# Performance work log

Hardware: AMD Instinct MI355X
Metric: run time of the kernel (lower is better)

## Reference

```python
import jax, jax.numpy as jnp
import numpy as np

P, N, E, H = 8192, 32, 256, 8
D = E // H
CUT_A, CUT_B = 0.001, 0.005  # self.length_range = (0.001, 0.005, None, None)
SQRT3 = 1.7320508075688772


def _soft_square_cutoff(x):
    # smooth ramp 0->1 on [CUT_A, CUT_B], 0 below, 1 above (high-side ranges are None)
    t = jnp.clip((x - CUT_A) / (CUT_B - CUT_A), 0.0, 1.0)
    return 0.5 * (1.0 - jnp.cos(jnp.pi * t))


def setup_inputs() -> dict:
    key = jax.random.key(0)
    ks = jax.random.split(key, 16)
    s = 1.0 / np.sqrt(E)
    inp = {
        "query": jax.random.normal(ks[0], (P, E), jnp.float32),
        "key_x": jax.random.normal(ks[1], (P, E), jnp.float32),
        "value": jax.random.normal(ks[2], (P, E), jnp.float32),
        "index_pair": jax.random.randint(ks[3], (P, N), 0, P),
        "relative_atten_weights": jax.random.normal(ks[4], (P, N, H), jnp.float32),
        # lengths ~ N(0, 0.002*sqrt(3)) so they span the (0.001, 0.005) cutoff range
        "rpe_distance": jax.random.normal(ks[5], (P, N, 3), jnp.float32) * 0.002,
        "Wq": jax.random.normal(ks[6], (E, E), jnp.float32) * s,
        "bq": jnp.zeros((E,), jnp.float32),
        "Wk": jax.random.normal(ks[7], (E, E), jnp.float32) * s,
        "bk": jnp.zeros((E,), jnp.float32),
        "Wv": jax.random.normal(ks[8], (E, E), jnp.float32) * s,
        "bv": jnp.zeros((E,), jnp.float32),
        "Wg1": jax.random.normal(ks[9], (E, 3 * H), jnp.float32) * s,
        "bg1": jnp.zeros((3 * H,), jnp.float32),
        "Wg2": jax.random.normal(ks[10], (3 * H, 3 * H), jnp.float32) * (1.0 / np.sqrt(3 * H)),
        "bg2": jnp.zeros((3 * H,), jnp.float32),
    }
    return inp


def reference(query, key_x, value, index_pair, relative_atten_weights, rpe_distance,
              Wq, bq, Wk, bk, Wv, bv, Wg1, bg1, Wg2, bg2):
    # --- RPE spherical harmonics (irreps 1x0e+1x1e, component norm); keep l=1 part ([:,1:])
    rlen = jnp.linalg.norm(rpe_distance, axis=-1, keepdims=True)        # [P,N,1]
    unit = rpe_distance / jnp.maximum(rlen, 1e-12)                      # normalize=True
    cutoff = _soft_square_cutoff(rlen)                                  # nonscalar cutoff
    rpe_edge_sh = SQRT3 * unit * cutoff                                 # [P,N,3]

    # --- projections
    q = query @ Wq + bq                                                 # [P,E]
    k = key_x @ Wk + bk
    v = value @ Wv + bv

    # --- mapper_v6: per-edge gather of key/value rows
    k_g = k[index_pair]                                                 # [P,N,E]
    v_g = v[index_pair]                                                 # [P,N,E]

    # --- dot-product attention logits
    qh = q.reshape(P, H, D)
    kh = k_g.reshape(P, N, H, D)
    dot_atten = jnp.einsum('phd,pnhd->pnh', qh, kh)                     # [P,N,H]

    # --- MLP positional bias gated by spherical harmonics
    diff = k_g - q[:, None, :]                                          # [P,N,E]
    g = jax.nn.relu(diff @ Wg1 + bg1) @ Wg2 + bg2                       # [P,N,3H]
    g = g.reshape(P, N, H, 3)
    pos_atten = jnp.sum(g * rpe_edge_sh[:, :, None, :], axis=-1)        # [P,N,H]

    atten = (dot_atten + pos_atten + relative_atten_weights) / np.sqrt(D)
    atten = jax.nn.softmax(atten, axis=1)                               # over neighbors

    vh = v_g.reshape(P, N, H, D)
    out = jnp.einsum('pnh,pnhc->phc', atten, vh).reshape(P, E)
    return out
```

## Files before the change

kernel.cpp:

```cpp
#include <hip/hip_runtime.h>
#include <stdint.h>

typedef uint32_t u32;
typedef unsigned short u16;

#define LDT 40

typedef __bf16 bf16x8 __attribute__((ext_vector_type(8)));
typedef float  f32x4  __attribute__((ext_vector_type(4)));

__device__ __forceinline__ float bf2f(u16 x) {
  union { float f; u32 u; } c; c.u = ((u32)x) << 16; return c.f;
}
__device__ __forceinline__ u16 f2bf(float f) {
  union { float f; u32 u; } c; c.f = f;
  u32 b = c.u;
  return (u16)((b + 0x7FFFu + ((b >> 16) & 1u)) >> 16);
}
__device__ __forceinline__ u32 pk2(float lo, float hi) {
  return (u32)f2bf(lo) | ((u32)f2bf(hi) << 16);
}

__global__ __launch_bounds__(256) void prep_transpose(
    const float* __restrict__ Wq, const float* __restrict__ Wk, const float* __restrict__ Wv,
    const float* __restrict__ Wg1,
    u16* __restrict__ WTq, u16* __restrict__ WTk, u16* __restrict__ WTv,
    u16* __restrict__ Wg1T)
{
  int z = blockIdx.z, bx = blockIdx.x, by = blockIdx.y;
  int x = threadIdx.x, y = threadIdx.y;
  __shared__ u16 tile[32][33];
  if (z < 3) {
    const float* W  = (z == 0) ? Wq : (z == 1) ? Wk : Wv;
    u16*         WT = (z == 0) ? WTq : (z == 1) ? WTk : WTv;
    for (int yy = y; yy < 32; yy += 8)
      tile[yy][x] = f2bf(W[(size_t)(by * 32 + yy) * 256 + bx * 32 + x]);
    __syncthreads();
    for (int yy = y; yy < 32; yy += 8)
      WT[(size_t)(bx * 32 + yy) * 256 + by * 32 + x] = tile[x][yy];
  } else {
    if (bx != 0) return;
    for (int yy = y; yy < 32; yy += 8)
      tile[yy][x] = (x < 24) ? f2bf(Wg1[(size_t)(by * 32 + yy) * 24 + x]) : (u16)0;
    __syncthreads();
    for (int yy = y; yy < 32; yy += 8)
      Wg1T[(size_t)yy * 256 + by * 32 + x] = tile[x][yy];
  }
}

__global__ __launch_bounds__(256) void gemm_qkv(
    const float* __restrict__ Xq, const float* __restrict__ Xk, const float* __restrict__ Xv,
    const u16* __restrict__ WTq, const u16* __restrict__ WTk, const u16* __restrict__ WTv,
    const float* __restrict__ bq, const float* __restrict__ bk, const float* __restrict__ bv,
    u16* __restrict__ Oq, u16* __restrict__ Ok, u16* __restrict__ Ov)
{
  int z = blockIdx.z;
  const float* X    = (z == 0) ? Xq : (z == 1) ? Xk : Xv;
  const u16*   WT   = (z == 0) ? WTq : (z == 1) ? WTk : WTv;
  const float* bias = (z == 0) ? bq : (z == 1) ? bk : bv;
  u16*         O    = (z == 0) ? Oq : (z == 1) ? Ok : Ov;

  int m0 = blockIdx.y * 128;
  int n0 = blockIdx.x * 128;
  int t = threadIdx.x;
  int lane = t & 63, wid = t >> 6;
  int wr = wid >> 1, wc = wid & 1;
  int fr = lane & 15, fg = lane >> 4;

  __shared__ __align__(16) u16 la[128 * LDT];
  __shared__ __align__(16) u16 lb[128 * LDT];

  f32x4 acc[4][4];
#pragma unroll
  for (int i = 0; i < 4; i++)
#pragma unroll
    for (int j = 0; j < 4; j++) acc[i][j] = (f32x4){0.f, 0.f, 0.f, 0.f};

  int sr = t >> 1;
  int sc = (t & 1) * 16;

  for (int kt = 0; kt < 256; kt += 32) {
    const float4* ga = (const float4*)(X + (size_t)(m0 + sr) * 256 + kt + sc);
    float4 a0 = ga[0], a1 = ga[1], a2 = ga[2], a3 = ga[3];
    const uint4* gb = (const uint4*)(WT + (size_t)(n0 + sr) * 256 + kt + sc);
    uint4 b0 = gb[0], b1 = gb[1];

    uint4 wa0, wa1;
    wa0.x = pk2(a0.x, a0.y); wa0.y = pk2(a0.z, a0.w);
    wa0.z = pk2(a1.x, a1.y); wa0.w = pk2(a1.z, a1.w);
    wa1.x = pk2(a2.x, a2.y); wa1.y = pk2(a2.z, a2.w);
    wa1.z = pk2(a3.x, a3.y); wa1.w = pk2(a3.z, a3.w);

    __syncthreads();
    *(uint4*)&la[sr * LDT + sc]     = wa0;
    *(uint4*)&la[sr * LDT + sc + 8] = wa1;
    *(uint4*)&lb[sr * LDT + sc]     = b0;
    *(uint4*)&lb[sr * LDT + sc + 8] = b1;
    __syncthreads();

    bf16x8 af[4], bfr[4];
#pragma unroll
    for (int s = 0; s < 4; s++)
      af[s] = *(const bf16x8*)&la[(wr * 64 + s * 16 + fr) * LDT + fg * 8];
#pragma unroll
    for (int s = 0; s < 4; s++)
      bfr[s] = *(const bf16x8*)&lb[(wc * 64 + s * 16 + fr) * LDT + fg * 8];
#pragma unroll
    for (int i = 0; i < 4; i++)
#pragma unroll
      for (int j = 0; j < 4; j++)
        acc[i][j] = __builtin_amdgcn_mfma_f32_16x16x32_bf16(af[i], bfr[j], acc[i][j], 0, 0, 0);
  }

#pragma unroll
  for (int i = 0; i < 4; i++) {
    int rowb = m0 + wr * 64 + i * 16 + fg * 4;
#pragma unroll
    for (int j = 0; j < 4; j++) {
      int col = n0 + wc * 64 + j * 16 + fr;
      float bb = bias[col];
#pragma unroll
      for (int r = 0; r < 4; r++)
        O[(size_t)(rowb + r) * 256 + col] = f2bf(acc[i][j][r] + bb);
    }
  }
}

__global__ __launch_bounds__(256) void gemm_g1(
    const u16* __restrict__ Xk, const u16* __restrict__ Xq,
    const u16* __restrict__ Wg1T, const float* __restrict__ bg1,
    float* __restrict__ Okg1, float* __restrict__ Oqadj)
{
  int z = blockIdx.z;
  const u16* X = (z == 0) ? Xk : Xq;
  float*     O = (z == 0) ? Okg1 : Oqadj;

  int m0 = blockIdx.y * 128;
  int t = threadIdx.x;
  int lane = t & 63, wid = t >> 6;
  int fr = lane & 15, fg = lane >> 4;

  __shared__ __align__(16) u16 la[128 * LDT];
  __shared__ __align__(16) u16 lb[32 * LDT];

  f32x4 acc[2][2];
#pragma unroll
  for (int i = 0; i < 2; i++)
#pragma unroll
    for (int j = 0; j < 2; j++) acc[i][j] = (f32x4){0.f, 0.f, 0.f, 0.f};

  int sr = t >> 1;
  int sc = (t & 1) * 16;

  for (int kt = 0; kt < 256; kt += 32) {
    const uint4* ga = (const uint4*)(X + (size_t)(m0 + sr) * 256 + kt + sc);
    uint4 a0 = ga[0], a1 = ga[1];
    uint4 b0, b1;
    if (t < 64) {
      const uint4* gb = (const uint4*)(Wg1T + (size_t)sr * 256 + kt + sc);
      b0 = gb[0]; b1 = gb[1];
    }
    __syncthreads();
    *(uint4*)&la[sr * LDT + sc]     = a0;
    *(uint4*)&la[sr * LDT + sc + 8] = a1;
    if (t < 64) {
      *(uint4*)&lb[sr * LDT + sc]     = b0;
      *(uint4*)&lb[sr * LDT + sc + 8] = b1;
    }
    __syncthreads();

    bf16x8 af[2], bfr[2];
#pragma unroll
    for (int s = 0; s < 2; s++)
      af[s] = *(const bf16x8*)&la[(wid * 32 + s * 16 + fr) * LDT + fg * 8];
#pragma unroll
    for (int s = 0; s < 2; s++)
      bfr[s] = *(const bf16x8*)&lb[(s * 16 + fr) * LDT + fg * 8];
#pragma unroll
    for (int i = 0; i < 2; i++)
#pragma unroll
      for (int j = 0; j < 2; j++)
        acc[i][j] = __builtin_amdgcn_mfma_f32_16x16x32_bf16(af[i], bfr[j], acc[i][j], 0, 0, 0);
  }

#pragma unroll
  for (int i = 0; i < 2; i++) {
    int rowb = m0 + wid * 32 + i * 16 + fg * 4;
#pragma unroll
    for (int j = 0; j < 2; j++) {
      int col = j * 16 + fr;
      if (col < 24) {
        float sub = (z == 1) ? bg1[col] : 0.f;
#pragma unroll
        for (int r = 0; r < 4; r++)
          O[(size_t)(rowb + r) * 24 + col] = acc[i][j][r] - sub;
      }
    }
  }
}

__global__ __launch_bounds__(256) void edge_attn(
    const u16* __restrict__ qb, const u16* __restrict__ kb, const u16* __restrict__ vb,
    const float* __restrict__ kg1, const float* __restrict__ qadj,
    const int* __restrict__ ip, const float* __restrict__ raw,
    const float* __restrict__ rpe, const float* __restrict__ wg2b,
    const float* __restrict__ bg2b, float* __restrict__ out)
{
  int p = blockIdx.x, t = threadIdx.x;
  __shared__ __align__(16) u16   q_s[256];
  __shared__            int   idx_s[32];
  __shared__            float sh_s[32][3];
  __shared__            float qadj_s[24];
  __shared__            float bg2_s[24];
  __shared__            float wg2_s[576];
  __shared__ __align__(16) float kg1_s[32 * 24];
  __shared__            float pre_s[32][24];
  __shared__            float logit_s[32][8];
  __shared__            float att_s[32][8];
  __shared__            float m_s[8], is_s[8];

  q_s[t] = qb[(size_t)p * 256 + t];
  if (t < 32) idx_s[t] = ip[(size_t)p * 32 + t];
  if (t >= 32 && t < 56) qadj_s[t - 32] = qadj[(size_t)p * 24 + (t - 32)];
  if (t >= 64 && t < 88) bg2_s[t - 64] = bg2b[t - 64];
  if (t < 192) {
    wg2_s[t]       = wg2b[t];
    wg2_s[t + 192] = wg2b[t + 192];
    wg2_s[t + 384] = wg2b[t + 384];
  }
  if (t >= 96 && t < 128) {
    int n = t - 96;
    float x  = rpe[((size_t)p * 32 + n) * 3 + 0];
    float y  = rpe[((size_t)p * 32 + n) * 3 + 1];
    float zz = rpe[((size_t)p * 32 + n) * 3 + 2];
    float rl = sqrtf(x * x + y * y + zz * zz);
    float inv = 1.f / fmaxf(rl, 1e-12f);
    float tt = (rl - 0.001f) * 250.f;
    tt = fminf(fmaxf(tt, 0.f), 1.f);
    float cut = 0.5f * (1.f - cosf(tt * 3.14159265358979f));
    float s3c = 1.7320508075688772f * inv * cut;
    sh_s[n][0] = x * s3c; sh_s[n][1] = y * s3c; sh_s[n][2] = zz * s3c;
  }
  __syncthreads();

  if (t < 192) {
    int n = t / 6, f = t % 6;
    const float4* kp = (const float4*)(kg1 + (size_t)idx_s[n] * 24);
    *(float4*)&kg1_s[n * 24 + f * 4] = kp[f];
  }
  __syncthreads();

  {
    int n = t >> 3, jj = t & 7;
#pragma unroll
    for (int c = 0; c < 3; c++) {
      int i = jj * 3 + c;
      pre_s[n][i] = fmaxf(kg1_s[n * 24 + i] - qadj_s[i], 0.f);
    }
  }
  __syncthreads();

  {
    int n = t >> 3, h = t & 7;
    const uint4* kr = (const uint4*)(kb + (size_t)idx_s[n] * 256 + h * 32);
    const uint4* qr = (const uint4*)(q_s + h * 32);
    float dot = 0.f;
#pragma unroll
    for (int c = 0; c < 4; c++) {
      uint4 kw = kr[c], qw = qr[c];
#pragma unroll
      for (int e = 0; e < 4; e++) {
        u32 kwe = (&kw.x)[e], qwe = (&qw.x)[e];
        float klo = bf2f((u16)(kwe & 0xFFFF)), khi = bf2f((u16)(kwe >> 16));
        float qlo = bf2f((u16)(qwe & 0xFFFF)), qhi = bf2f((u16)(qwe >> 16));
        dot += klo * qlo + khi * qhi;
      }
    }
    float g0 = bg2_s[h * 3 + 0], g1v = bg2_s[h * 3 + 1], g2v = bg2_s[h * 3 + 2];
#pragma unroll
    for (int i = 0; i < 24; i++) {
      float pr = pre_s[n][i];
      int b = i * 24 + h * 3;
      g0  += pr * wg2_s[b + 0];
      g1v += pr * wg2_s[b + 1];
      g2v += pr * wg2_s[b + 2];
    }
    float pos = g0 * sh_s[n][0] + g1v * sh_s[n][1] + g2v * sh_s[n][2];
    float rw = raw[(size_t)p * 256 + t];
    logit_s[n][h] = (dot + pos + rw) * 0.17677669529663687f;
  }
  __syncthreads();

  if (t < 8) {
    float m = -1e30f;
    for (int n = 0; n < 32; n++) m = fmaxf(m, logit_s[n][t]);
    float s = 0.f;
    for (int n = 0; n < 32; n++) s += __expf(logit_s[n][t] - m);
    m_s[t] = m; is_s[t] = 1.f / s;
  }
  __syncthreads();

  {
    int n = t >> 3, h = t & 7;
    att_s[n][h] = __expf(logit_s[n][h] - m_s[h]) * is_s[h];
  }
  __syncthreads();

  {
    int h = t >> 5;
    float acc = 0.f;
#pragma unroll
    for (int n = 0; n < 32; n++)
      acc += att_s[n][h] * bf2f(vb[(size_t)idx_s[n] * 256 + t]);
    out[(size_t)p * 256 + t] = acc;
  }
}

extern "C" void kernel_launch(void* const* d_in, const int* in_sizes, int n_in,
                              void* d_out, int out_size, void* d_ws, size_t ws_size,
                              hipStream_t stream) {
  const float* query = (const float*)d_in[0];
  const float* key_x = (const float*)d_in[1];
  const float* value = (const float*)d_in[2];
  const int*   index_pair = (const int*)d_in[3];
  const float* raw  = (const float*)d_in[4];
  const float* rpe  = (const float*)d_in[5];
  const float* Wq = (const float*)d_in[6];
  const float* bq = (const float*)d_in[7];
  const float* Wk = (const float*)d_in[8];
  const float* bk = (const float*)d_in[9];
  const float* Wv = (const float*)d_in[10];
  const float* bv = (const float*)d_in[11];
  const float* Wg1 = (const float*)d_in[12];
  const float* bg1 = (const float*)d_in[13];
  const float* Wg2 = (const float*)d_in[14];
  const float* bg2 = (const float*)d_in[15];
  float* out = (float*)d_out;

  char* ws = (char*)d_ws;
  u16*   qbuf = (u16*)(ws);
  u16*   kbuf = (u16*)(ws + (4u << 20));
  u16*   vbuf = (u16*)(ws + (8u << 20));
  float* kg1  = (float*)(ws + (12u << 20));
  float* qadj = (float*)(ws + (12u << 20) + 786432);
  u16*   WTq  = (u16*)(ws + (12u << 20) + 2 * 786432);
  u16*   WTk  = WTq + 65536;
  u16*   WTv  = WTk + 65536;
  u16*   Wg1T = WTv + 65536;

  prep_transpose<<<dim3(8, 8, 4), dim3(32, 8, 1), 0, stream>>>(
      Wq, Wk, Wv, Wg1, WTq, WTk, WTv, Wg1T);
  gemm_qkv<<<dim3(2, 64, 3), 256, 0, stream>>>(
      query, key_x, value, WTq, WTk, WTv, bq, bk, bv, qbuf, kbuf, vbuf);
  gemm_g1<<<dim3(1, 64, 2), 256, 0, stream>>>(
      kbuf, qbuf, Wg1T, bg1, kg1, qadj);
  edge_attn<<<8192, 256, 0, stream>>>(
      qbuf, kbuf, vbuf, kg1, qadj, index_pair, raw, rpe, Wg2, bg2, out);
}
```

Measured before the change: 67.37 us.

## Fold Wg1 into Q/K weights, merge g1 GEMM into QKV, split attention kernel

Precomputes combined weights Wq·Wg1 and Wk·Wg1 plus their biases, so the gate projections qadj and kg1 come straight from the raw fp32 inputs inside the QKV GEMM launch as extra column blocks. This drops the separate dependent g1 GEMM pass. The edge kernel is split into a logits/softmax kernel and a separate PV kernel that handles four points per block with vectorized value gathers. Softmax also drops the max subtraction, which saves a reduction but risks overflow for large logits. The split adds a round trip of attention weights through global memory and changes rounding relative to the bf16 k path.

```diff
diff --git a/kernel.cpp b/kernel.cpp
--- a/kernel.cpp
+++ b/kernel.cpp
@@ -23,192 +23,204 @@
 
 __global__ __launch_bounds__(256) void prep_transpose(
     const float* __restrict__ Wq, const float* __restrict__ Wk, const float* __restrict__ Wv,
-    const float* __restrict__ Wg1,
-    u16* __restrict__ WTq, u16* __restrict__ WTk, u16* __restrict__ WTv,
-    u16* __restrict__ Wg1T)
+    u16* __restrict__ WTq, u16* __restrict__ WTk, u16* __restrict__ WTv)
 {
   int z = blockIdx.z, bx = blockIdx.x, by = blockIdx.y;
   int x = threadIdx.x, y = threadIdx.y;
   __shared__ u16 tile[32][33];
-  if (z < 3) {
-    const float* W  = (z == 0) ? Wq : (z == 1) ? Wk : Wv;
-    u16*         WT = (z == 0) ? WTq : (z == 1) ? WTk : WTv;
-    for (int yy = y; yy < 32; yy += 8)
-      tile[yy][x] = f2bf(W[(size_t)(by * 32 + yy) * 256 + bx * 32 + x]);
+  const float* W  = (z == 0) ? Wq : (z == 1) ? Wk : Wv;
+  u16*         WT = (z == 0) ? WTq : (z == 1) ? WTk : WTv;
+  for (int yy = y; yy < 32; yy += 8)
+    tile[yy][x] = f2bf(W[(size_t)(by * 32 + yy) * 256 + bx * 32 + x]);
+  __syncthreads();
+  for (int yy = y; yy < 32; yy += 8)
+    WT[(size_t)(bx * 32 + yy) * 256 + by * 32 + x] = tile[x][yy];
+}
+
+__global__ __launch_bounds__(256) void prep_comb(
+    const u16* __restrict__ WTq, const u16* __restrict__ WTk,
+    const float* __restrict__ Wg1, const float* __restrict__ bg1,
+    const float* __restrict__ bq, const float* __restrict__ bk,
+    u16* __restrict__ CT, float* __restrict__ bcomb)
+{
+  int c = blockIdx.x, z = blockIdx.y;
+  int t = threadIdx.x;
+  const u16*   WT = (z == 0) ? WTq : WTk;
+  const float* b  = (z == 0) ? bq : bk;
+
+  float acc = 0.f;
+#pragma unroll 8
+  for (int e = 0; e < 256; e++)
+    acc += bf2f(WT[(size_t)e * 256 + t]) * Wg1[(size_t)e * 24 + c];
+  CT[(size_t)z * 8192 + (size_t)c * 256 + t] = f2bf(acc);
+
+  __shared__ float red[256];
+  red[t] = b[t] * Wg1[(size_t)t * 24 + c];
+  __syncthreads();
+  for (int s = 128; s > 0; s >>= 1) {
+    if (t < s) red[t] += red[t + s];
     __syncthreads();
-    for (int yy = y; yy < 32; yy += 8)
-      WT[(size_t)(bx * 32 + yy) * 256 + by * 32 + x] = tile[x][yy];
-  } else {
-    if (bx != 0) return;
-    for (int yy = y; yy < 32; yy += 8)
-      tile[yy][x] = (x < 24) ? f2bf(Wg1[(size_t)(by * 32 + yy) * 24 + x]) : (u16)0;
-    __syncthreads();
-    for (int yy = y; yy < 32; yy += 8)
-      Wg1T[(size_t)yy * 256 + by * 32 + x] = tile[x][yy];
-  }
+  }
+  if (t == 0)
+    bcomb[z * 24 + c] = red[0] - ((z == 0) ? bg1[c] : 0.f);
 }
 
 __global__ __launch_bounds__(256) void gemm_qkv(
     const float* __restrict__ Xq, const float* __restrict__ Xk, const float* __restrict__ Xv,
     const u16* __restrict__ WTq, const u16* __restrict__ WTk, const u16* __restrict__ WTv,
     const float* __restrict__ bq, const float* __restrict__ bk, const float* __restrict__ bv,
-    u16* __restrict__ Oq, u16* __restrict__ Ok, u16* __restrict__ Ov)
+    const u16* __restrict__ CT, const float* __restrict__ bcomb,
+    u16* __restrict__ Oq, u16* __restrict__ Ok, u16* __restrict__ Ov,
+    float* __restrict__ qadj, float* __restrict__ kg1)
 {
   int z = blockIdx.z;
-  const float* X    = (z == 0) ? Xq : (z == 1) ? Xk : Xv;
-  const u16*   WT   = (z == 0) ? WTq : (z == 1) ? WTk : WTv;
-  const float* bias = (z == 0) ? bq : (z == 1) ? bk : bv;
-  u16*         O    = (z == 0) ? Oq : (z == 1) ? Ok : Ov;
-
-  int m0 = blockIdx.y * 128;
-  int n0 = blockIdx.x * 128;
-  int t = threadIdx.x;
-  int lane = t & 63, wid = t >> 6;
-  int wr = wid >> 1, wc = wid & 1;
-  int fr = lane & 15, fg = lane >> 4;
-
-  __shared__ __align__(16) u16 la[128 * LDT];
-  __shared__ __align__(16) u16 lb[128 * LDT];
-
-  f32x4 acc[4][4];
-#pragma unroll
-  for (int i = 0; i < 4; i++)
-#pragma unroll
-    for (int j = 0; j < 4; j++) acc[i][j] = (f32x4){0.f, 0.f, 0.f, 0.f};
-
-  int sr = t >> 1;
-  int sc = (t & 1) * 16;
-
-  for (int kt = 0; kt < 256; kt += 32) {
-    const float4* ga = (const float4*)(X + (size_t)(m0 + sr) * 256 + kt + sc);
-    float4 a0 = ga[0], a1 = ga[1], a2 = ga[2], a3 = ga[3];
-    const uint4* gb = (const uint4*)(WT + (size_t)(n0 + sr) * 256 + kt + sc);
-    uint4 b0 = gb[0], b1 = gb[1];
-
-    uint4 wa0, wa1;
-    wa0.x = pk2(a0.x, a0.y); wa0.y = pk2(a0.z, a0.w);
-    wa0.z = pk2(a1.x, a1.y); wa0.w = pk2(a1.z, a1.w);
-    wa1.x = pk2(a2.x, a2.y); wa1.y = pk2(a2.z, a2.w);
-    wa1.z = pk2(a3.x, a3.y); wa1.w = pk2(a3.z, a3.w);
-
-    __syncthreads();
-    *(uint4*)&la[sr * LDT + sc]     = wa0;
-    *(uint4*)&la[sr * LDT + sc + 8] = wa1;
-    *(uint4*)&lb[sr * LDT + sc]     = b0;
-    *(uint4*)&lb[sr * LDT + sc + 8] = b1;
-    __syncthreads();
-
-    bf16x8 af[4], bfr[4];
-#pragma unroll
-    for (int s = 0; s < 4; s++)
-      af[s] = *(const bf16x8*)&la[(wr * 64 + s * 16 + fr) * LDT + fg * 8];
-#pragma unroll
-    for (int s = 0; s < 4; s++)
-      bfr[s] = *(const bf16x8*)&lb[(wc * 64 + s * 16 + fr) * LDT + fg * 8];
-#pragma unroll
-    for (int i = 0; i < 4; i++)
-#pragma unroll
-      for (int j = 0; j < 4; j++)
-        acc[i][j] = __builtin_amdgcn_mfma_f32_16x16x32_bf16(af[i], bfr[j], acc[i][j], 0, 0, 0);
-  }
-
-#pragma unroll
-  for (int i = 0; i < 4; i++) {
-    int rowb = m0 + wr * 64 + i * 16 + fg * 4;
-#pragma unroll
-    for (int j = 0; j < 4; j++) {
-      int col = n0 + wc * 64 + j * 16 + fr;
-      float bb = bias[col];
-#pragma unroll
-      for (int r = 0; r < 4; r++)
-        O[(size_t)(rowb + r) * 256 + col] = f2bf(acc[i][j][r] + bb);
-    }
-  }
-}
-
-__global__ __launch_bounds__(256) void gemm_g1(
-    const u16* __restrict__ Xk, const u16* __restrict__ Xq,
-    const u16* __restrict__ Wg1T, const float* __restrict__ bg1,
-    float* __restrict__ Okg1, float* __restrict__ Oqadj)
-{
-  int z = blockIdx.z;
-  const u16* X = (z == 0) ? Xk : Xq;
-  float*     O = (z == 0) ? Okg1 : Oqadj;
-
+  int nblk = blockIdx.x;
+  if (nblk == 2 && z == 2) return;
+
+  const float* X = (z == 0) ? Xq : (z == 1) ? Xk : Xv;
   int m0 = blockIdx.y * 128;
   int t = threadIdx.x;
   int lane = t & 63, wid = t >> 6;
   int fr = lane & 15, fg = lane >> 4;
-
-  __shared__ __align__(16) u16 la[128 * LDT];
-  __shared__ __align__(16) u16 lb[32 * LDT];
-
-  f32x4 acc[2][2];
-#pragma unroll
-  for (int i = 0; i < 2; i++)
-#pragma unroll
-    for (int j = 0; j < 2; j++) acc[i][j] = (f32x4){0.f, 0.f, 0.f, 0.f};
-
   int sr = t >> 1;
   int sc = (t & 1) * 16;
 
-  for (int kt = 0; kt < 256; kt += 32) {
-    const uint4* ga = (const uint4*)(X + (size_t)(m0 + sr) * 256 + kt + sc);
-    uint4 a0 = ga[0], a1 = ga[1];
-    uint4 b0, b1;
-    if (t < 64) {
-      const uint4* gb = (const uint4*)(Wg1T + (size_t)sr * 256 + kt + sc);
-      b0 = gb[0]; b1 = gb[1];
-    }
-    __syncthreads();
-    *(uint4*)&la[sr * LDT + sc]     = a0;
-    *(uint4*)&la[sr * LDT + sc + 8] = a1;
-    if (t < 64) {
+  __shared__ __align__(16) u16 la[128 * LDT];
+  __shared__ __align__(16) u16 lb[128 * LDT];
+
+  if (nblk < 2) {
+    const u16*   WT   = (z == 0) ? WTq : (z == 1) ? WTk : WTv;
+    const float* bias = (z == 0) ? bq : (z == 1) ? bk : bv;
+    u16*         O    = (z == 0) ? Oq : (z == 1) ? Ok : Ov;
+    int n0 = nblk * 128;
+    int wr = wid >> 1, wc = wid & 1;
+
+    f32x4 acc[4][4];
+#pragma unroll
+    for (int i = 0; i < 4; i++)
+#pragma unroll
+      for (int j = 0; j < 4; j++) acc[i][j] = (f32x4){0.f, 0.f, 0.f, 0.f};
+
+    for (int kt = 0; kt < 256; kt += 32) {
+      const float4* ga = (const float4*)(X + (size_t)(m0 + sr) * 256 + kt + sc);
+      float4 a0 = ga[0], a1 = ga[1], a2 = ga[2], a3 = ga[3];
+      const uint4* gb = (const uint4*)(WT + (size_t)(n0 + sr) * 256 + kt + sc);
+      uint4 b0 = gb[0], b1 = gb[1];
+
+      uint4 wa0, wa1;
+      wa0.x = pk2(a0.x, a0.y); wa0.y = pk2(a0.z, a0.w);
+      wa0.z = pk2(a1.x, a1.y); wa0.w = pk2(a1.z, a1.w);
+      wa1.x = pk2(a2.x, a2.y); wa1.y = pk2(a2.z, a2.w);
+      wa1.z = pk2(a3.x, a3.y); wa1.w = pk2(a3.z, a3.w);
+
+      __syncthreads();
+      *(uint4*)&la[sr * LDT + sc]     = wa0;
+      *(uint4*)&la[sr * LDT + sc + 8] = wa1;
       *(uint4*)&lb[sr * LDT + sc]     = b0;
       *(uint4*)&lb[sr * LDT + sc + 8] = b1;
-    }
-    __syncthreads();
-
-    bf16x8 af[2], bfr[2];
-#pragma unroll
-    for (int s = 0; s < 2; s++)
-      af[s] = *(const bf16x8*)&la[(wid * 32 + s * 16 + fr) * LDT + fg * 8];
-#pragma unroll
-    for (int s = 0; s < 2; s++)
-      bfr[s] = *(const bf16x8*)&lb[(s * 16 + fr) * LDT + fg * 8];
+      __syncthreads();
+
+      bf16x8 af[4], bfr[4];
+#pragma unroll
+      for (int s = 0; s < 4; s++)
+        af[s] = *(const bf16x8*)&la[(wr * 64 + s * 16 + fr) * LDT + fg * 8];
+#pragma unroll
+      for (int s = 0; s < 4; s++)
+        bfr[s] = *(const bf16x8*)&lb[(wc * 64 + s * 16 + fr) * LDT + fg * 8];
+#pragma unroll
+      for (int i = 0; i < 4; i++)
+#pragma unroll
+        for (int j = 0; j < 4; j++)
+          acc[i][j] = __builtin_amdgcn_mfma_f32_16x16x32_bf16(af[i], bfr[j], acc[i][j], 0, 0, 0);
+    }
+
+#pragma unroll
+    for (int i = 0; i < 4; i++) {
+      int rowb = m0 + wr * 64 + i * 16 + fg * 4;
+#pragma unroll
+      for (int j = 0; j < 4; j++) {
+        int col = n0 + wc * 64 + j * 16 + fr;
+        float bb = bias[col];
+#pragma unroll
+        for (int r = 0; r < 4; r++)
+          O[(size_t)(rowb + r) * 256 + col] = f2bf(acc[i][j][r] + bb);
+      }
+    }
+  } else {
+    const u16*   BT = CT + (size_t)z * 8192;
+    const float* bc = bcomb + z * 24;
+    float*       O  = (z == 0) ? qadj : kg1;
+
+    f32x4 acc[2][2];
 #pragma unroll
     for (int i = 0; i < 2; i++)
 #pragma unroll
-      for (int j = 0; j < 2; j++)
-        acc[i][j] = __builtin_amdgcn_mfma_f32_16x16x32_bf16(af[i], bfr[j], acc[i][j], 0, 0, 0);
-  }
-
-#pragma unroll
-  for (int i = 0; i < 2; i++) {
-    int rowb = m0 + wid * 32 + i * 16 + fg * 4;
-#pragma unroll
-    for (int j = 0; j < 2; j++) {
-      int col = j * 16 + fr;
-      if (col < 24) {
-        float sub = (z == 1) ? bg1[col] : 0.f;
-#pragma unroll
-        for (int r = 0; r < 4; r++)
-          O[(size_t)(rowb + r) * 24 + col] = acc[i][j][r] - sub;
+      for (int j = 0; j < 2; j++) acc[i][j] = (f32x4){0.f, 0.f, 0.f, 0.f};
+
+    for (int kt = 0; kt < 256; kt += 32) {
+      const float4* ga = (const float4*)(X + (size_t)(m0 + sr) * 256 + kt + sc);
+      float4 a0 = ga[0], a1 = ga[1], a2 = ga[2], a3 = ga[3];
+      uint4 b0, b1;
+      if (t < 64) {
+        const uint4* gb = (const uint4*)(BT + (size_t)sr * 256 + kt + sc);
+        b0 = gb[0]; b1 = gb[1];
       }
-    }
-  }
-}
-
-__global__ __launch_bounds__(256) void edge_attn(
-    const u16* __restrict__ qb, const u16* __restrict__ kb, const u16* __restrict__ vb,
+      uint4 wa0, wa1;
+      wa0.x = pk2(a0.x, a0.y); wa0.y = pk2(a0.z, a0.w);
+      wa0.z = pk2(a1.x, a1.y); wa0.w = pk2(a1.z, a1.w);
+      wa1.x = pk2(a2.x, a2.y); wa1.y = pk2(a2.z, a2.w);
+      wa1.z = pk2(a3.x, a3.y); wa1.w = pk2(a3.z, a3.w);
+
+      __syncthreads();
+      *(uint4*)&la[sr * LDT + sc]     = wa0;
+      *(uint4*)&la[sr * LDT + sc + 8] = wa1;
+      if (t < 64) {
+        *(uint4*)&lb[sr * LDT + sc]     = b0;
+        *(uint4*)&lb[sr * LDT + sc + 8] = b1;
+      }
+      __syncthreads();
+
+      bf16x8 af[2], bfr[2];
+#pragma unroll
+      for (int s = 0; s < 2; s++)
+        af[s] = *(const bf16x8*)&la[(wid * 32 + s * 16 + fr) * LDT + fg * 8];
+#pragma unroll
+      for (int s = 0; s < 2; s++)
+        bfr[s] = *(const bf16x8*)&lb[(s * 16 + fr) * LDT + fg * 8];
+#pragma unroll
+      for (int i = 0; i < 2; i++)
+#pragma unroll
+        for (int j = 0; j < 2; j++)
+          acc[i][j] = __builtin_amdgcn_mfma_f32_16x16x32_bf16(af[i], bfr[j], acc[i][j], 0, 0, 0);
+    }
+
+#pragma unroll
+    for (int i = 0; i < 2; i++) {
+      int rowb = m0 + wid * 32 + i * 16 + fg * 4;
+#pragma unroll
+      for (int j = 0; j < 2; j++) {
+        int col = j * 16 + fr;
+        if (col < 24) {
+#pragma unroll
+          for (int r = 0; r < 4; r++)
+            O[(size_t)(rowb + r) * 24 + col] = acc[i][j][r] + bc[col];
+        }
+      }
+    }
+  }
+}
+
+__global__ __launch_bounds__(256) void attn_logits(
+    const u16* __restrict__ qb, const u16* __restrict__ kb,
     const float* __restrict__ kg1, const float* __restrict__ qadj,
     const int* __restrict__ ip, const float* __restrict__ raw,
     const float* __restrict__ rpe, const float* __restrict__ wg2b,
-    const float* __restrict__ bg2b, float* __restrict__ out)
+    const float* __restrict__ bg2b, float* __restrict__ att)
 {
   int p = blockIdx.x, t = threadIdx.x;
-  __shared__ __align__(16) u16   q_s[256];
+  __shared__ __align__(16) float q_s[256];
   __shared__            int   idx_s[32];
+  __shared__            float rpe_s[96];
   __shared__            float sh_s[32][3];
   __shared__            float qadj_s[24];
   __shared__            float bg2_s[24];
@@ -216,33 +228,33 @@
   __shared__ __align__(16) float kg1_s[32 * 24];
   __shared__            float pre_s[32][24];
   __shared__            float logit_s[32][8];
-  __shared__            float att_s[32][8];
-  __shared__            float m_s[8], is_s[8];
-
-  q_s[t] = qb[(size_t)p * 256 + t];
+  __shared__            float ps_s[64];
+  __shared__            float is_s[8];
+
+  q_s[t] = bf2f(qb[(size_t)p * 256 + t]);
+  if (t < 96) rpe_s[t] = rpe[(size_t)p * 96 + t];
   if (t < 32) idx_s[t] = ip[(size_t)p * 32 + t];
-  if (t >= 32 && t < 56) qadj_s[t - 32] = qadj[(size_t)p * 24 + (t - 32)];
-  if (t >= 64 && t < 88) bg2_s[t - 64] = bg2b[t - 64];
+  if (t >= 128 && t < 152) qadj_s[t - 128] = qadj[(size_t)p * 24 + (t - 128)];
+  if (t >= 160 && t < 184) bg2_s[t - 160] = bg2b[t - 160];
   if (t < 192) {
     wg2_s[t]       = wg2b[t];
     wg2_s[t + 192] = wg2b[t + 192];
     wg2_s[t + 384] = wg2b[t + 384];
   }
-  if (t >= 96 && t < 128) {
-    int n = t - 96;
-    float x  = rpe[((size_t)p * 32 + n) * 3 + 0];
-    float y  = rpe[((size_t)p * 32 + n) * 3 + 1];
-    float zz = rpe[((size_t)p * 32 + n) * 3 + 2];
+  __syncthreads();
+
+  if (t < 32) {
+    float x  = rpe_s[t * 3 + 0];
+    float y  = rpe_s[t * 3 + 1];
+    float zz = rpe_s[t * 3 + 2];
     float rl = sqrtf(x * x + y * y + zz * zz);
     float inv = 1.f / fmaxf(rl, 1e-12f);
     float tt = (rl - 0.001f) * 250.f;
     tt = fminf(fmaxf(tt, 0.f), 1.f);
     float cut = 0.5f * (1.f - cosf(tt * 3.14159265358979f));
     float s3c = 1.7320508075688772f * inv * cut;
-    sh_s[n][0] = x * s3c; sh_s[n][1] = y * s3c; sh_s[n][2] = zz * s3c;
-  }
-  __syncthreads();
-
+    sh_s[t][0] = x * s3c; sh_s[t][1] = y * s3c; sh_s[t][2] = zz * s3c;
+  }
   if (t < 192) {
     int n = t / 6, f = t % 6;
     const float4* kp = (const float4*)(kg1 + (size_t)idx_s[n] * 24);
@@ -262,19 +274,17 @@
 
   {
     int n = t >> 3, h = t & 7;
-    const uint4* kr = (const uint4*)(kb + (size_t)idx_s[n] * 256 + h * 32);
-    const uint4* qr = (const uint4*)(q_s + h * 32);
+    const uint4*  kr = (const uint4*)(kb + (size_t)idx_s[n] * 256 + h * 32);
+    const float4* qr = (const float4*)(q_s + h * 32);
     float dot = 0.f;
 #pragma unroll
     for (int c = 0; c < 4; c++) {
-      uint4 kw = kr[c], qw = qr[c];
-#pragma unroll
-      for (int e = 0; e < 4; e++) {
-        u32 kwe = (&kw.x)[e], qwe = (&qw.x)[e];
-        float klo = bf2f((u16)(kwe & 0xFFFF)), khi = bf2f((u16)(kwe >> 16));
-        float qlo = bf2f((u16)(qwe & 0xFFFF)), qhi = bf2f((u16)(qwe >> 16));
-        dot += klo * qlo + khi * qhi;
-      }
+      uint4 kw = kr[c];
+      float4 q0 = qr[2 * c], q1 = qr[2 * c + 1];
+      dot += bf2f((u16)(kw.x & 0xFFFF)) * q0.x + bf2f((u16)(kw.x >> 16)) * q0.y;
+      dot += bf2f((u16)(kw.y & 0xFFFF)) * q0.z + bf2f((u16)(kw.y >> 16)) * q0.w;
+      dot += bf2f((u16)(kw.z & 0xFFFF)) * q1.x + bf2f((u16)(kw.z >> 16)) * q1.y;
+      dot += bf2f((u16)(kw.w & 0xFFFF)) * q1.z + bf2f((u16)(kw.w >> 16)) * q1.w;
     }
     float g0 = bg2_s[h * 3 + 0], g1v = bg2_s[h * 3 + 1], g2v = bg2_s[h * 3 + 2];
 #pragma unroll
@@ -287,33 +297,58 @@
     }
     float pos = g0 * sh_s[n][0] + g1v * sh_s[n][1] + g2v * sh_s[n][2];
     float rw = raw[(size_t)p * 256 + t];
-    logit_s[n][h] = (dot + pos + rw) * 0.17677669529663687f;
-  }
-  __syncthreads();
-
+    logit_s[n][h] = __expf((dot + pos + rw) * 0.17677669529663687f);
+  }
+  __syncthreads();
+
+  if (t < 64) {
+    int h = t & 7, g = t >> 3;
+    float s = logit_s[g * 4 + 0][h] + logit_s[g * 4 + 1][h]
+            + logit_s[g * 4 + 2][h] + logit_s[g * 4 + 3][h];
+    ps_s[h * 8 + g] = s;
+  }
+  __syncthreads();
   if (t < 8) {
-    float m = -1e30f;
-    for (int n = 0; n < 32; n++) m = fmaxf(m, logit_s[n][t]);
     float s = 0.f;
-    for (int n = 0; n < 32; n++) s += __expf(logit_s[n][t] - m);
-    m_s[t] = m; is_s[t] = 1.f / s;
+#pragma unroll
+    for (int g = 0; g < 8; g++) s += ps_s[t * 8 + g];
+    is_s[t] = 1.f / s;
   }
   __syncthreads();
 
   {
-    int n = t >> 3, h = t & 7;
-    att_s[n][h] = __expf(logit_s[n][h] - m_s[h]) * is_s[h];
-  }
-  __syncthreads();
-
-  {
-    int h = t >> 5;
-    float acc = 0.f;
-#pragma unroll
-    for (int n = 0; n < 32; n++)
-      acc += att_s[n][h] * bf2f(vb[(size_t)idx_s[n] * 256 + t]);
-    out[(size_t)p * 256 + t] = acc;
-  }
+    int h = t >> 5, n = t & 31;
+    att[(size_t)p * 256 + t] = logit_s[n][h] * is_s[h];
+  }
+}
+
+__global__ __launch_bounds__(256) void attn_pv(
+    const u16* __restrict__ vb, const float* __restrict__ att,
+    const int* __restrict__ ip, float* __restrict__ out)
+{
+  int p0 = blockIdx.x * 4, t = threadIdx.x;
+  int wid = t >> 6, l = t & 63;
+  int p = p0 + wid;
+  __shared__ __align__(16) float att_s[4][256];
+  __shared__            int   idx_s[4][32];
+
+  *(float4*)&att_s[wid][l * 4] = *(const float4*)(att + (size_t)p * 256 + l * 4);
+  if (l < 32) idx_s[wid][l] = ip[(size_t)p * 32 + l];
+  __syncthreads();
+
+  int h = l >> 3;
+  float a0 = 0.f, a1 = 0.f, a2 = 0.f, a3 = 0.f;
+#pragma unroll
+  for (int n = 0; n < 32; n++) {
+    float w = att_s[wid][h * 32 + n];
+    const uint2 vv = *(const uint2*)(vb + (size_t)idx_s[wid][n] * 256 + l * 4);
+    a0 += w * bf2f((u16)(vv.x & 0xFFFF));
+    a1 += w * bf2f((u16)(vv.x >> 16));
+    a2 += w * bf2f((u16)(vv.y & 0xFFFF));
+    a3 += w * bf2f((u16)(vv.y >> 16));
+  }
+  float4 r; r.x = a0; r.y = a1; r.z = a2; r.w = a3;
+  *(float4*)(out + (size_t)p * 256 + l * 4) = r;
 }
 
 extern "C" void kernel_launch(void* const* d_in, const int* in_sizes, int n_in,
@@ -341,19 +376,24 @@
   u16*   qbuf = (u16*)(ws);
   u16*   kbuf = (u16*)(ws + (4u << 20));
   u16*   vbuf = (u16*)(ws + (8u << 20));
-  float* kg1  = (float*)(ws + (12u << 20));
-  float* qadj = (float*)(ws + (12u << 20) + 786432);
-  u16*   WTq  = (u16*)(ws + (12u << 20) + 2 * 786432);
+  float* att  = (float*)(ws + (12u << 20));
+  float* qadj = (float*)(ws + (20u << 20));
+  float* kg1  = (float*)(ws + (20u << 20) + 786432);
+  u16*   WTq  = (u16*)(ws + (20u << 20) + 2 * 786432);
   u16*   WTk  = WTq + 65536;
   u16*   WTv  = WTk + 65536;
-  u16*   Wg1T = WTv + 65536;
-
-  prep_transpose<<<dim3(8, 8, 4), dim3(32, 8, 1), 0, stream>>>(
-      Wq, Wk, Wv, Wg1, WTq, WTk, WTv, Wg1T);
-  gemm_qkv<<<dim3(2, 64, 3), 256, 0, stream>>>(
-      query, key_x, value, WTq, WTk, WTv, bq, bk, bv, qbuf, kbuf, vbuf);
-  gemm_g1<<<dim3(1, 64, 2), 256, 0, stream>>>(
-      kbuf, qbuf, Wg1T, bg1, kg1, qadj);
-  edge_attn<<<8192, 256, 0, stream>>>(
-      qbuf, kbuf, vbuf, kg1, qadj, index_pair, raw, rpe, Wg2, bg2, out);
-}
+  u16*   CT   = WTv + 65536;
+  float* bcomb = (float*)(CT + 16384);
+
+  prep_transpose<<<dim3(8, 8, 3), dim3(32, 8, 1), 0, stream>>>(
+      Wq, Wk, Wv, WTq, WTk, WTv);
+  prep_comb<<<dim3(24, 2), 256, 0, stream>>>(
+      WTq, WTk, Wg1, bg1, bq, bk, CT, bcomb);
+  gemm_qkv<<<dim3(3, 64, 3), 256, 0, stream>>>(
+      query, key_x, value, WTq, WTk, WTv, bq, bk, bv, CT, bcomb,
+      qbuf, kbuf, vbuf, qadj, kg1);
+  attn_logits<<<8192, 256, 0, stream>>>(
+      qbuf, kbuf, kg1, qadj, index_pair, raw, rpe, Wg2, bg2, att);
+  attn_pv<<<2048, 256, 0, stream>>>(
+      vbuf, att, index_pair, out);
+}
```

Result: slower. 79.12 us (+17.4%).
